# Optimization experiments

Hardware: AMD Instinct MI355X
Metric: run time of the kernel (lower is better)

The kernel has to match this reference:

```python
import jax, jax.numpy as jnp
import numpy as np

# db4 decomposition low-pass filter, pywt coefficient order
DEC_LO = np.array([-0.010597401784997278, 0.032883011666982945,
                   0.030841381835986965, -0.18703481171888114,
                   -0.02798376941698385, 0.6308807679295904,
                   0.7148465705525415, 0.23037781330885523], dtype=np.float32)
LEVEL = 5
B, C, L = 64, 64, 8192


def _qmf_hi(dec_lo):
    # pywt relation: dec_hi[n] = (-1)^(n+1) * dec_lo[F-1-n]
    F = dec_lo.shape[0]
    signs = jnp.where(jnp.arange(F) % 2 == 0, -1.0, 1.0).astype(dec_lo.dtype)
    return signs * dec_lo[::-1]


def _wavedec(x, dec_lo, dec_hi):
    # pywt.dwt(v, w, 'symmetric') == np.convolve(sym_pad(v, F-1), filt, 'valid')[1::2]
    # implemented as a stride-2 cross-correlation with the reversed filter.
    b, c, n = x.shape
    v = x.reshape(b * c, n)
    F = dec_lo.shape[0]
    # kernel: (out_ch=2 [lo, hi], in_ch=1, width=F); reversed => true convolution
    k = jnp.stack([dec_lo[::-1], dec_hi[::-1]])[:, None, :]
    details = []
    for _ in range(LEVEL):
        ext = jnp.pad(v, ((0, 0), (F - 1, F - 1)), mode='symmetric')[:, 1:]
        y = jax.lax.conv_general_dilated(ext[:, None, :], k,
                                         window_strides=(2,), padding='VALID')
        v = y[:, 0, :]           # approximation -> next level input
        details.append(y[:, 1, :])  # detail for this level (finest first)
    approx = v.reshape(b, c, -1)
    # pywt order: [cA_L, cD_L, ..., cD_1] -> coarsest detail first
    det = [d.reshape(b, c, -1) for d in reversed(details)]
    return (approx, *det)


def setup_inputs() -> dict:
    key = jax.random.key(0)
    x = jax.random.normal(key, (B, C, L), dtype=jnp.float32)
    dec_lo = jnp.asarray(DEC_LO)
    dec_hi = _qmf_hi(dec_lo)
    return {"x": x, "dec_lo": dec_lo, "dec_hi": dec_hi}


def reference(x, dec_lo, dec_hi):
    # Returns (cA_L, cD_L, cD_{L-1}, ..., cD_1), matching the torch module's
    # [approx_tensor, detail_tensors] flattened.
    return _wavedec(x, dec_lo, dec_hi)
```

## Files before the change

kernel.cpp:

```cpp
#include <hip/hip_runtime.h>


static constexpr int ROWS = 4096;
static constexpr int N0 = 8192;
static constexpr int L1n = 4099, L2n = 2053, L3n = 1030, L4n = 518, L5n = 262;
static constexpr size_t OFF_D5 = 1073152u;
static constexpr size_t OFF_D4 = 2146304u;
static constexpr size_t OFF_D3 = 4268032u;
static constexpr size_t OFF_D2 = 8486912u;
static constexpr size_t OFF_D1 = 16896000u;

template <int STRIDE, int UNROLL>
__device__ __forceinline__ void dwt_level(
    const float* __restrict__ src, int n, int m,
    const float* __restrict__ h, const float* __restrict__ g,
    float* __restrict__ adst, float* __restrict__ ddst, int tid)
{
    const int ngroups = (m + 3) >> 2;
    const int jmax = (n - 10) >> 3;
#pragma unroll UNROLL
    for (int j = tid; j < ngroups; j += STRIDE) {
        const int p0 = 4 * j;
        if (j >= 1 && j <= jmax && p0 + 3 < m) {
            const float2* __restrict__ s2 =
                reinterpret_cast<const float2*>(src) + (4 * j - 3);
            float w[16];
#pragma unroll
            for (int t = 0; t < 8; ++t) {
                const float2 v = s2[t];
                w[2 * t] = v.x; w[2 * t + 1] = v.y;
            }
            float aa[4], dd[4];
#pragma unroll
            for (int r = 0; r < 4; ++r) {
                float a = 0.f, d = 0.f;
#pragma unroll
                for (int q = 0; q < 8; ++q) {
                    const float v = w[2 * r + 7 - q];
                    a = fmaf(h[q], v, a);
                    d = fmaf(g[q], v, d);
                }
                aa[r] = a; dd[r] = d;
            }
#pragma unroll
            for (int r = 0; r < 4; ++r) ddst[p0 + r] = dd[r];
#pragma unroll
            for (int r = 0; r < 4; ++r) adst[p0 + r] = aa[r];
        } else {
#pragma unroll 4
            for (int r = 0; r < 4; ++r) {
                const int pos = p0 + r;
                if (pos >= m) break;
                const int s0 = 2 * pos + 1;
                float a = 0.f, d = 0.f;
#pragma unroll
                for (int q = 0; q < 8; ++q) {
                    int s = s0 - q;
                    int idx = (s < 0) ? (-1 - s) : ((s >= n) ? (2 * n - 1 - s) : s);
                    const float v = src[idx];
                    a = fmaf(h[q], v, a);
                    d = fmaf(g[q], v, d);
                }
                ddst[pos] = d;
                adst[pos] = a;
            }
        }
    }
}

__global__ __launch_bounds__(512, 3)
void wavedec5_kernel(const float* __restrict__ x,
                     const float* __restrict__ dlo,
                     const float* __restrict__ dhi,
                     float* __restrict__ out)
{
    __shared__ __align__(16) float bufA[2][4100];
    __shared__ __align__(16) float bufB[2][2056];

    const int half = threadIdx.x >> 8;
    const int tid  = threadIdx.x & 255;
    const int row  = (blockIdx.x << 1) + half;

    float h[8], g[8];
#pragma unroll
    for (int i = 0; i < 8; ++i) { h[i] = dlo[i]; g[i] = dhi[i]; }

    const float* __restrict__ xr = x + (size_t)row * N0;
    float* __restrict__ bA = bufA[half];
    float* __restrict__ bB = bufB[half];

    dwt_level<256, 2>(xr, N0, L1n, h, g, bA,
                      out + OFF_D1 + (size_t)row * L1n, tid);
    __syncthreads();
    dwt_level<256, 1>(bA, L1n, L2n, h, g, bB,
                      out + OFF_D2 + (size_t)row * L2n, tid);
    __syncthreads();
    dwt_level<256, 1>(bB, L2n, L3n, h, g, bA,
                      out + OFF_D3 + (size_t)row * L3n, tid);
    __syncthreads();
    dwt_level<256, 1>(bA, L3n, L4n, h, g, bB,
                      out + OFF_D4 + (size_t)row * L4n, tid);
    __syncthreads();
    dwt_level<256, 1>(bB, L4n, L5n, h, g,
                      out + (size_t)row * L5n,
                      out + OFF_D5 + (size_t)row * L5n, tid);
}

extern "C" void kernel_launch(void* const* d_in, const int* in_sizes, int n_in,
                              void* d_out, int out_size, void* d_ws, size_t ws_size,
                              hipStream_t stream) {
    const float* x   = (const float*)d_in[0];
    const float* dlo = (const float*)d_in[1];
    const float* dhi = (const float*)d_in[2];
    float* out = (float*)d_out;
    wavedec5_kernel<<<ROWS / 2, 512, 0, stream>>>(x, dlo, dhi, out);
}
```

Baseline: 63.85 us.

## Fuse DWT levels 1 and 2 in registers via wavefront shuffles, one row per block

Computes level-2 coefficients directly from level-1 approximation values held in registers, exchanging neighbours with wavefront shuffles and recomputing the values at wave boundaries from the input. This removes the level-1 shared-memory buffer, one barrier and one round of LDS traffic. Launch changes to one row per 256-thread block with smaller shared memory so more blocks fit per CU. The trade-off is redundant recomputation for lanes 0-1 and more complex boundary handling, which is error-prone.

```diff
diff --git a/kernel.cpp b/kernel.cpp
--- a/kernel.cpp
+++ b/kernel.cpp
@@ -10,7 +10,20 @@
 static constexpr size_t OFF_D2 = 8486912u;
 static constexpr size_t OFF_D1 = 16896000u;
 
-template <int STRIDE, int UNROLL>
+__device__ __forceinline__ float refl_load(const float* __restrict__ s, int idx, int n) {
+    int i = (idx < 0) ? (-1 - idx) : ((idx >= n) ? (2 * n - 1 - idx) : idx);
+    return s[i];
+}
+
+__device__ __forceinline__ float a1_val(const float* __restrict__ xr, int i,
+                                        const float* __restrict__ h) {
+    float a = 0.f;
+#pragma unroll
+    for (int q = 0; q < 8; ++q)
+        a = fmaf(h[q], refl_load(xr, 2 * i + 1 - q, N0), a);
+    return a;
+}
+
 __device__ __forceinline__ void dwt_level(
     const float* __restrict__ src, int n, int m,
     const float* __restrict__ h, const float* __restrict__ g,
@@ -18,8 +31,7 @@
 {
     const int ngroups = (m + 3) >> 2;
     const int jmax = (n - 10) >> 3;
-#pragma unroll UNROLL
-    for (int j = tid; j < ngroups; j += STRIDE) {
+    for (int j = tid; j < ngroups; j += 256) {
         const int p0 = 4 * j;
         if (j >= 1 && j <= jmax && p0 + 3 < m) {
             const float2* __restrict__ s2 =
@@ -30,7 +42,6 @@
                 const float2 v = s2[t];
                 w[2 * t] = v.x; w[2 * t + 1] = v.y;
             }
-            float aa[4], dd[4];
 #pragma unroll
             for (int r = 0; r < 4; ++r) {
                 float a = 0.f, d = 0.f;
@@ -40,12 +51,9 @@
                     a = fmaf(h[q], v, a);
                     d = fmaf(g[q], v, d);
                 }
-                aa[r] = a; dd[r] = d;
+                ddst[p0 + r] = d;
+                adst[p0 + r] = a;
             }
-#pragma unroll
-            for (int r = 0; r < 4; ++r) ddst[p0 + r] = dd[r];
-#pragma unroll
-            for (int r = 0; r < 4; ++r) adst[p0 + r] = aa[r];
         } else {
 #pragma unroll 4
             for (int r = 0; r < 4; ++r) {
@@ -55,9 +63,7 @@
                 float a = 0.f, d = 0.f;
 #pragma unroll
                 for (int q = 0; q < 8; ++q) {
-                    int s = s0 - q;
-                    int idx = (s < 0) ? (-1 - s) : ((s >= n) ? (2 * n - 1 - s) : s);
-                    const float v = src[idx];
+                    const float v = refl_load(src, s0 - q, n);
                     a = fmaf(h[q], v, a);
                     d = fmaf(g[q], v, d);
                 }
@@ -68,42 +74,118 @@
     }
 }
 
-__global__ __launch_bounds__(512, 3)
-void wavedec5_kernel(const float* __restrict__ x,
-                     const float* __restrict__ dlo,
-                     const float* __restrict__ dhi,
-                     float* __restrict__ out)
+__global__ __launch_bounds__(256, 8)
+void wavedec5_fused(const float* __restrict__ x,
+                    const float* __restrict__ dlo,
+                    const float* __restrict__ dhi,
+                    float* __restrict__ out)
 {
-    __shared__ __align__(16) float bufA[2][4100];
-    __shared__ __align__(16) float bufB[2][2056];
+    __shared__ __align__(16) float a2buf[2056];
+    __shared__ __align__(16) float a3buf[1032];
 
-    const int half = threadIdx.x >> 8;
-    const int tid  = threadIdx.x & 255;
-    const int row  = (blockIdx.x << 1) + half;
+    const int tid  = threadIdx.x;
+    const int lane = tid & 63;
+    const int row  = blockIdx.x;
 
     float h[8], g[8];
 #pragma unroll
     for (int i = 0; i < 8; ++i) { h[i] = dlo[i]; g[i] = dhi[i]; }
 
     const float* __restrict__ xr = x + (size_t)row * N0;
-    float* __restrict__ bA = bufA[half];
-    float* __restrict__ bB = bufB[half];
+    float* __restrict__ d1out = out + OFF_D1 + (size_t)row * L1n;
+    float* __restrict__ d2out = out + OFF_D2 + (size_t)row * L2n;
 
-    dwt_level<256, 2>(xr, N0, L1n, h, g, bA,
-                      out + OFF_D1 + (size_t)row * L1n, tid);
+    for (int j = 3 + tid; j <= 1022; j += 256) {
+        const float2* __restrict__ s2 =
+            reinterpret_cast<const float2*>(xr) + (4 * j - 3);
+        float w[16];
+#pragma unroll
+        for (int t = 0; t < 8; ++t) {
+            const float2 v = s2[t];
+            w[2 * t] = v.x; w[2 * t + 1] = v.y;
+        }
+        float a1o[4], dd[4];
+#pragma unroll
+        for (int r = 0; r < 4; ++r) {
+            float a = 0.f, d = 0.f;
+#pragma unroll
+            for (int q = 0; q < 8; ++q) {
+                const float v = w[2 * r + 7 - q];
+                a = fmaf(h[q], v, a);
+                d = fmaf(g[q], v, d);
+            }
+            a1o[r] = a; dd[r] = d;
+        }
+#pragma unroll
+        for (int r = 0; r < 4; ++r) d1out[4 * j + r] = dd[r];
+
+        float v0 = __shfl_up(a1o[2], 2, 64);
+        float v1 = __shfl_up(a1o[3], 2, 64);
+        float v2 = __shfl_up(a1o[0], 1, 64);
+        float v3 = __shfl_up(a1o[1], 1, 64);
+        float v4 = __shfl_up(a1o[2], 1, 64);
+        float v5 = __shfl_up(a1o[3], 1, 64);
+        if (lane < 2) {
+            v0 = a1_val(xr, 4 * j - 6, h);
+            v1 = a1_val(xr, 4 * j - 5, h);
+            v2 = a1_val(xr, 4 * j - 4, h);
+            v3 = a1_val(xr, 4 * j - 3, h);
+            v4 = a1_val(xr, 4 * j - 2, h);
+            v5 = a1_val(xr, 4 * j - 1, h);
+        }
+        float v[10] = {v0, v1, v2, v3, v4, v5, a1o[0], a1o[1], a1o[2], a1o[3]};
+        float a20 = 0.f, d20 = 0.f, a21 = 0.f, d21 = 0.f;
+#pragma unroll
+        for (int q = 0; q < 8; ++q) {
+            a20 = fmaf(h[q], v[7 - q], a20);
+            d20 = fmaf(g[q], v[7 - q], d20);
+            a21 = fmaf(h[q], v[9 - q], a21);
+            d21 = fmaf(g[q], v[9 - q], d21);
+        }
+        a2buf[2 * j]     = a20;
+        a2buf[2 * j + 1] = a21;
+        d2out[2 * j]     = d20;
+        d2out[2 * j + 1] = d21;
+    }
+
+    if (tid < 13) {
+        const int p = (tid < 6) ? tid : (2040 + tid);
+        float a2v = 0.f, d2v = 0.f;
+#pragma unroll
+        for (int q = 0; q < 8; ++q) {
+            int s = 2 * p + 1 - q;
+            int si = (s < 0) ? (-1 - s) : ((s >= L1n) ? (2 * L1n - 1 - s) : s);
+            const float av = a1_val(xr, si, h);
+            a2v = fmaf(h[q], av, a2v);
+            d2v = fmaf(g[q], av, d2v);
+        }
+        a2buf[p] = a2v;
+        d2out[p] = d2v;
+    } else if (tid < 18) {
+        const int j = (tid == 16) ? 1023 : ((tid == 17) ? 1024 : (tid - 13));
+#pragma unroll 4
+        for (int r = 0; r < 4; ++r) {
+            const int pos = 4 * j + r;
+            if (pos >= L1n) break;
+            const int s0 = 2 * pos + 1;
+            float d = 0.f;
+#pragma unroll
+            for (int q = 0; q < 8; ++q)
+                d = fmaf(g[q], refl_load(xr, s0 - q, N0), d);
+            d1out[pos] = d;
+        }
+    }
     __syncthreads();
-    dwt_level<256, 1>(bA, L1n, L2n, h, g, bB,
-                      out + OFF_D2 + (size_t)row * L2n, tid);
+
+    dwt_level(a2buf, L2n, L3n, h, g, a3buf,
+              out + OFF_D3 + (size_t)row * L3n, tid);
     __syncthreads();
-    dwt_level<256, 1>(bB, L2n, L3n, h, g, bA,
-                      out + OFF_D3 + (size_t)row * L3n, tid);
+    dwt_level(a3buf, L3n, L4n, h, g, a2buf,
+              out + OFF_D4 + (size_t)row * L4n, tid);
     __syncthreads();
-    dwt_level<256, 1>(bA, L3n, L4n, h, g, bB,
-                      out + OFF_D4 + (size_t)row * L4n, tid);
-    __syncthreads();
-    dwt_level<256, 1>(bB, L4n, L5n, h, g,
-                      out + (size_t)row * L5n,
-                      out + OFF_D5 + (size_t)row * L5n, tid);
+    dwt_level(a2buf, L4n, L5n, h, g,
+              out + (size_t)row * L5n,
+              out + OFF_D5 + (size_t)row * L5n, tid);
 }
 
 extern "C" void kernel_launch(void* const* d_in, const int* in_sizes, int n_in,
@@ -113,5 +195,5 @@
     const float* dlo = (const float*)d_in[1];
     const float* dhi = (const float*)d_in[2];
     float* out = (float*)d_out;
-    wavedec5_kernel<<<ROWS / 2, 512, 0, stream>>>(x, dlo, dhi, out);
+    wavedec5_fused<<<ROWS, 256, 0, stream>>>(x, dlo, dhi, out);
 }
```

Measured after the change: 78.84 us. 23.5% more time.
